# Kernel tuning notes

Hardware: AMD Instinct MI355X
Metric: run time of the kernel (lower is better)

Reference implementation:

```python
import jax, jax.numpy as jnp
import numpy as np

NUM_TERMS = 3
HIDDEN = 64
CLAMP_MIN = 1e-10


def _hermite_basis(x, num_terms):
    hs = [jnp.ones_like(x)]
    if num_terms > 1:
        hs.append(2.0 * x)
    for n in range(1, num_terms - 1):
        hs.append(2.0 * x * hs[n] - 2.0 * n * hs[n - 1])
    return jnp.stack(hs[:num_terms], axis=-1)  # (..., num_terms)


def setup_inputs() -> dict:
    key = jax.random.key(0)
    ks = jax.random.split(key, 7)
    B, S = 2048, 1024
    ys_coeffs = jax.random.normal(ks[0], (B, S, 2), dtype=jnp.float32)
    # scoring MLP params: Linear(3,64) -> ReLU -> Linear(64,64) -> ReLU -> Linear(64,num_terms)
    def lin(k, fan_in, fan_out):
        bound = 1.0 / np.sqrt(fan_in)
        kw, kb = jax.random.split(k)
        W = jax.random.uniform(kw, (fan_in, fan_out), minval=-bound, maxval=bound, dtype=jnp.float32)
        b = jax.random.uniform(kb, (fan_out,), minval=-bound, maxval=bound, dtype=jnp.float32)
        return W, b
    W1, b1 = lin(ks[1], 3, HIDDEN)
    W2, b2 = lin(ks[2], HIDDEN, HIDDEN)
    Wout, bout = lin(ks[3], HIDDEN, NUM_TERMS)
    return {"ys_coeffs": ys_coeffs, "W1": W1, "b1": b1, "W2": W2, "b2": b2,
            "Wout": Wout, "bout": bout}


def reference(ys_coeffs, W1, b1, W2, b2, Wout, bout):
    B, S, _ = ys_coeffs.shape
    timestamps = ys_coeffs[:, :, 0]
    values = ys_coeffs[:, :, 1]
    x0 = values[:, :-1]            # (B, S-1)
    xt = values[:, 1:]             # (B, S-1)
    t = timestamps[:, 1:]          # (B, S-1)
    feats = jnp.stack([xt, t, x0], axis=-1)           # (B, S-1, 3)
    h1 = jax.nn.relu(feats @ W1 + b1)                 # (B, S-1, 64)
    h2 = jax.nn.relu(h1 @ W2 + b2)                    # (B, S-1, 64)
    c_n = h2 @ Wout + bout                            # (B, S-1, num_terms)
    herm = _hermite_basis(xt, NUM_TERMS)              # (B, S-1, num_terms)
    p = jnp.sum(c_n * herm, axis=-1)                  # (B, S-1)
    p = jax.nn.softmax(p, axis=0)                     # softmax over batch dim (as in torch dim=0)
    log_likelihood = jnp.log(jnp.clip(p, CLAMP_MIN)).sum(axis=-1)  # (B,)
    return log_likelihood.mean()
```

## Files before the change

### kernel.cpp

```cpp
#include <hip/hip_runtime.h>
#include <hip/hip_bf16.h>

#define HIDDEN 64
#define BATCH 2048
#define SFULL 1024
#define SM1 1023
#define LN_CLAMP -23.025850929940457f
#define SP_PER 16

typedef __bf16 bf16x8 __attribute__((ext_vector_type(8)));
typedef float  f32x4  __attribute__((ext_vector_type(4)));
typedef float  f32x16 __attribute__((ext_vector_type(16)));

#define FRAG_UNITS 22

__device__ __forceinline__ int sig(int rg) {
    return 16 * ((rg >> 3) & 3) + 8 * ((rg >> 2) & 1) + (rg & 3) + 4 * (rg >> 5);
}

__global__ __launch_bounds__(256) void frag_setup_kernel(
    const float* __restrict__ W1, const float* __restrict__ b1,
    const float* __restrict__ W2, const float* __restrict__ b2,
    const float* __restrict__ Wout, char* __restrict__ F)
{
    const int l    = threadIdx.x & 63;
    const int wv   = threadIdx.x >> 6;
    const int pcol = l & 31;
    const int hi   = l >> 5;

    if (wv == 0) {
#pragma unroll
        for (int mt = 0; mt < 2; ++mt) {
            const int hout = sig(32 * mt + pcol);
            bf16x8 v;
#pragma unroll
            for (int j = 0; j < 8; ++j) {
                const int k = 8 * hi + j;
                v[j] = (k < 3) ? (__bf16)W1[k * 64 + hout]
                     : (k == 3) ? (__bf16)b1[hout] : (__bf16)0.0f;
            }
            *(bf16x8*)(F + ((mt * 64 + l) << 4)) = v;
        }
#pragma unroll
        for (int c = 0; c < 4; ++c) {
            bf16x8 v;
#pragma unroll
            for (int j = 0; j < 8; ++j) {
                const int k = 16 * c + 8 * hi + j;
                v[j] = (pcol < 3) ? (__bf16)Wout[k * 3 + pcol] : (__bf16)0.0f;
            }
            *(bf16x8*)(F + (((10 + c) * 64 + l) << 4)) = v;
        }
    } else if (wv == 1 || wv == 2) {
        const int mt = wv - 1;
        const int hout = sig(32 * mt + pcol);
#pragma unroll
        for (int c = 0; c < 4; ++c) {
            bf16x8 v;
#pragma unroll
            for (int j = 0; j < 8; ++j)
                v[j] = (__bf16)W2[(16 * c + 8 * hi + j) * 64 + hout];
            *(bf16x8*)(F + (((2 + mt * 4 + c) * 64 + l) << 4)) = v;
        }
    } else {
#pragma unroll
        for (int mt = 0; mt < 2; ++mt)
#pragma unroll
            for (int q = 0; q < 4; ++q) {
                f32x4 v;
#pragma unroll
                for (int rr = 0; rr < 4; ++rr) {
                    const int r = 4 * q + rr;
                    v[rr] = b2[16 * (r >> 2) + 8 * hi + (r & 3) + 4 * mt];
                }
                *(f32x4*)(F + (((14 + mt * 4 + q) * 64 + l) << 4)) = v;
            }
    }
}

__global__ __launch_bounds__(256, 3) void mlp_z_kernel(
    const float* __restrict__ ys,
    const char* __restrict__ F,
    const float* __restrict__ bout,
    float* __restrict__ z)
{
    const int l    = threadIdx.x & 63;
    const int wv   = threadIdx.x >> 6;
    const int pcol = l & 31;

    const int b   = (blockIdx.x * 4 + wv) * 32 + pcol;
    const int sp0 = blockIdx.y * SP_PER;
    const int omax = (SFULL - 1) - sp0;

    bf16x8 a1[2], a2[2][4], a3[4];
    f32x16 c2init[2];
#pragma unroll
    for (int mt = 0; mt < 2; ++mt) {
        a1[mt] = *(const bf16x8*)(F + ((mt * 64 + l) << 4));
#pragma unroll
        for (int c = 0; c < 4; ++c)
            a2[mt][c] = *(const bf16x8*)(F + (((2 + mt * 4 + c) * 64 + l) << 4));
#pragma unroll
        for (int q = 0; q < 4; ++q) {
            const f32x4 v = *(const f32x4*)(F + (((14 + mt * 4 + q) * 64 + l) << 4));
            c2init[mt][4 * q + 0] = v[0]; c2init[mt][4 * q + 1] = v[1];
            c2init[mt][4 * q + 2] = v[2]; c2init[mt][4 * q + 3] = v[3];
        }
    }
#pragma unroll
    for (int c = 0; c < 4; ++c)
        a3[c] = *(const bf16x8*)(F + (((10 + c) * 64 + l) << 4));

    const float bo0 = bout[0], bo1 = bout[1], bo2 = bout[2];

    f32x16 zero16;
#pragma unroll
    for (int i = 0; i < 16; ++i) zero16[i] = 0.0f;

    const float2* base2 = reinterpret_cast<const float2*>(ys) + ((size_t)b * SFULL + sp0);
    float* zb = z + (size_t)sp0 * BATCH + b;

    float2 q0 = base2[0];
    float2 q1 = base2[min(1, omax)];
    float2 qn = base2[min(2, omax)];

    for (int it = 0; it < SP_PER; ++it) {
        const float2 qn2 = base2[min(it + 3, omax)];

        const float x0 = q0.y, t = q1.x, xt = q1.y;

        bf16x8 f0;
        f0[0] = (__bf16)xt; f0[1] = (__bf16)t;
        f0[2] = (__bf16)x0; f0[3] = (__bf16)1.0f;
        f0[4] = f0[0]; f0[5] = f0[1]; f0[6] = f0[2]; f0[7] = f0[3];

        f32x16 acc1_0 = __builtin_amdgcn_mfma_f32_32x32x16_bf16(a1[0], f0, zero16, 0, 0, 0);
        f32x16 acc1_1 = __builtin_amdgcn_mfma_f32_32x32x16_bf16(a1[1], f0, zero16, 0, 0, 0);

        bf16x8 h1f[4];
#pragma unroll
        for (int c = 0; c < 4; ++c)
#pragma unroll
            for (int j = 0; j < 4; ++j) {
                h1f[c][j]     = (__bf16)fmaxf(acc1_0[4 * c + j], 0.0f);
                h1f[c][4 + j] = (__bf16)fmaxf(acc1_1[4 * c + j], 0.0f);
            }

        f32x16 acc2_0 = c2init[0];
        f32x16 acc2_1 = c2init[1];
#pragma unroll
        for (int c = 0; c < 4; ++c) {
            acc2_0 = __builtin_amdgcn_mfma_f32_32x32x16_bf16(a2[0][c], h1f[c], acc2_0, 0, 0, 0);
            acc2_1 = __builtin_amdgcn_mfma_f32_32x32x16_bf16(a2[1][c], h1f[c], acc2_1, 0, 0, 0);
        }

        bf16x8 h2f[4];
#pragma unroll
        for (int c = 0; c < 4; ++c)
#pragma unroll
            for (int j = 0; j < 4; ++j) {
                h2f[c][j]     = (__bf16)fmaxf(acc2_0[4 * c + j], 0.0f);
                h2f[c][4 + j] = (__bf16)fmaxf(acc2_1[4 * c + j], 0.0f);
            }

        f32x16 acc3 = zero16;
#pragma unroll
        for (int c = 0; c < 4; ++c)
            acc3 = __builtin_amdgcn_mfma_f32_32x32x16_bf16(a3[c], h2f[c], acc3, 0, 0, 0);

        const float c0 = acc3[0] + bo0;
        const float c1 = acc3[1] + bo1;
        const float c2 = acc3[2] + bo2;
        const float zv = fmaf(c2, fmaf(4.0f * xt, xt, -2.0f),
                         fmaf(c1, xt + xt, c0));

        if (l < 32 && sp0 + it < SM1)
            zb[(size_t)it * BATCH] = zv;

        q0 = q1; q1 = qn; qn = qn2;
    }
}

__device__ __forceinline__ float blk_reduce_max(float v) {
    __shared__ float s[4];
#pragma unroll
    for (int off = 32; off >= 1; off >>= 1) v = fmaxf(v, __shfl_xor(v, off));
    if ((threadIdx.x & 63) == 0) s[threadIdx.x >> 6] = v;
    __syncthreads();
    v = fmaxf(fmaxf(s[0], s[1]), fmaxf(s[2], s[3]));
    __syncthreads();
    return v;
}

__device__ __forceinline__ float blk_reduce_sum(float v) {
    __shared__ float s[4];
#pragma unroll
    for (int off = 32; off >= 1; off >>= 1) v += __shfl_xor(v, off);
    if ((threadIdx.x & 63) == 0) s[threadIdx.x >> 6] = v;
    __syncthreads();
    v = (s[0] + s[1]) + (s[2] + s[3]);
    __syncthreads();
    return v;
}

__global__ __launch_bounds__(256) void col_softmax_kernel(
    const float* __restrict__ z, float* __restrict__ colsum)
{
    const int sp = blockIdx.x;
    const int tid = threadIdx.x;
    const float* col = z + (size_t)sp * BATCH;

    float vals[8];
    float m = -3.4e38f;
#pragma unroll
    for (int i = 0; i < 8; ++i) {
        vals[i] = col[tid + 256 * i];
        m = fmaxf(m, vals[i]);
    }
    const float M = blk_reduce_max(m);

    float se = 0.0f;
#pragma unroll
    for (int i = 0; i < 8; ++i) se += __expf(vals[i] - M);
    const float S = blk_reduce_sum(se);
    const float L = __logf(S);

    float acc = 0.0f;
#pragma unroll
    for (int i = 0; i < 8; ++i) acc += fmaxf(vals[i] - M - L, LN_CLAMP);
    const float T = blk_reduce_sum(acc);
    if (tid == 0) colsum[sp] = T;
}

__global__ __launch_bounds__(256) void final_reduce_kernel(
    const float* __restrict__ colsum, float* __restrict__ out)
{
    const int tid = threadIdx.x;
    float v = 0.0f;
    for (int i = tid; i < SM1; i += 256) v += colsum[i];
    const float T = blk_reduce_sum(v);
    if (tid == 0) out[0] = T / (float)BATCH;
}

extern "C" void kernel_launch(void* const* d_in, const int* in_sizes, int n_in,
                              void* d_out, int out_size, void* d_ws, size_t ws_size,
                              hipStream_t stream) {
    const float* ys   = (const float*)d_in[0];
    const float* W1   = (const float*)d_in[1];
    const float* b1   = (const float*)d_in[2];
    const float* W2   = (const float*)d_in[3];
    const float* b2   = (const float*)d_in[4];
    const float* Wout = (const float*)d_in[5];
    const float* bout = (const float*)d_in[6];
    float* out = (float*)d_out;

    float* z      = (float*)d_ws;
    float* colsum = z + (size_t)SM1 * BATCH;
    size_t fo = ((size_t)SM1 * BATCH + SM1) * sizeof(float);
    fo = (fo + 15) & ~(size_t)15;
    char* F = (char*)d_ws + fo;

    frag_setup_kernel<<<1, 256, 0, stream>>>(W1, b1, W2, b2, Wout, F);
    dim3 grid1(16, 64);
    mlp_z_kernel<<<grid1, 256, 0, stream>>>(ys, F, bout, z);
    col_softmax_kernel<<<SM1, 256, 0, stream>>>(z, colsum);
    final_reduce_kernel<<<1, 256, 0, stream>>>(colsum, out);
}
```

Measured before the change: 48.69 us.

## Interleave two timesteps per iteration and pack bf16 with byte-permute truncation

```diff
diff --git a/kernel.cpp b/kernel.cpp
--- a/kernel.cpp
+++ b/kernel.cpp
@@ -6,7 +6,7 @@
 #define SFULL 1024
 #define SM1 1023
 #define LN_CLAMP -23.025850929940457f
-#define SP_PER 16
+#define PAIRS 8
 
 typedef __bf16 bf16x8 __attribute__((ext_vector_type(8)));
 typedef float  f32x4  __attribute__((ext_vector_type(4)));
@@ -16,6 +16,33 @@
 
 __device__ __forceinline__ int sig(int rg) {
     return 16 * ((rg >> 3) & 3) + 8 * ((rg >> 2) & 1) + (rg & 3) + 4 * (rg >> 5);
+}
+
+__device__ __forceinline__ unsigned pkt(float lo, float hi) {
+    return __builtin_amdgcn_perm(__float_as_uint(hi), __float_as_uint(lo), 0x07060302u);
+}
+__device__ __forceinline__ unsigned rp2(float lo, float hi) {
+    return pkt(fmaxf(lo, 0.0f), fmaxf(hi, 0.0f));
+}
+
+__device__ __forceinline__ void relu_pack4(const f32x16 lo, const f32x16 hi, bf16x8* out) {
+#pragma unroll
+    for (int c = 0; c < 4; ++c) {
+        union { unsigned u[4]; bf16x8 v; } r;
+        r.u[0] = rp2(lo[4 * c + 0], lo[4 * c + 1]);
+        r.u[1] = rp2(lo[4 * c + 2], lo[4 * c + 3]);
+        r.u[2] = rp2(hi[4 * c + 0], hi[4 * c + 1]);
+        r.u[3] = rp2(hi[4 * c + 2], hi[4 * c + 3]);
+        out[c] = r.v;
+    }
+}
+
+__device__ __forceinline__ bf16x8 featpk(float xt, float t, float x0) {
+    union { unsigned u[4]; bf16x8 v; } r;
+    r.u[0] = pkt(xt, t);
+    r.u[1] = pkt(x0, 1.0f);
+    r.u[2] = r.u[0]; r.u[3] = r.u[1];
+    return r.v;
 }
 
 __global__ __launch_bounds__(256) void frag_setup_kernel(
@@ -78,7 +105,7 @@
     }
 }
 
-__global__ __launch_bounds__(256, 3) void mlp_z_kernel(
+__global__ __launch_bounds__(256, 2) void mlp_z_kernel(
     const float* __restrict__ ys,
     const char* __restrict__ F,
     const float* __restrict__ bout,
@@ -89,7 +116,7 @@
     const int pcol = l & 31;
 
     const int b   = (blockIdx.x * 4 + wv) * 32 + pcol;
-    const int sp0 = blockIdx.y * SP_PER;
+    const int sp0 = blockIdx.y * (2 * PAIRS);
     const int omax = (SFULL - 1) - sp0;
 
     bf16x8 a1[2], a2[2][4], a3[4];
@@ -120,64 +147,66 @@
     const float2* base2 = reinterpret_cast<const float2*>(ys) + ((size_t)b * SFULL + sp0);
     float* zb = z + (size_t)sp0 * BATCH + b;
 
-    float2 q0 = base2[0];
-    float2 q1 = base2[min(1, omax)];
-    float2 qn = base2[min(2, omax)];
-
-    for (int it = 0; it < SP_PER; ++it) {
-        const float2 qn2 = base2[min(it + 3, omax)];
-
-        const float x0 = q0.y, t = q1.x, xt = q1.y;
-
-        bf16x8 f0;
-        f0[0] = (__bf16)xt; f0[1] = (__bf16)t;
-        f0[2] = (__bf16)x0; f0[3] = (__bf16)1.0f;
-        f0[4] = f0[0]; f0[5] = f0[1]; f0[6] = f0[2]; f0[7] = f0[3];
-
-        f32x16 acc1_0 = __builtin_amdgcn_mfma_f32_32x32x16_bf16(a1[0], f0, zero16, 0, 0, 0);
-        f32x16 acc1_1 = __builtin_amdgcn_mfma_f32_32x32x16_bf16(a1[1], f0, zero16, 0, 0, 0);
-
-        bf16x8 h1f[4];
-#pragma unroll
-        for (int c = 0; c < 4; ++c)
-#pragma unroll
-            for (int j = 0; j < 4; ++j) {
-                h1f[c][j]     = (__bf16)fmaxf(acc1_0[4 * c + j], 0.0f);
-                h1f[c][4 + j] = (__bf16)fmaxf(acc1_1[4 * c + j], 0.0f);
-            }
-
-        f32x16 acc2_0 = c2init[0];
-        f32x16 acc2_1 = c2init[1];
-#pragma unroll
-        for (int c = 0; c < 4; ++c) {
-            acc2_0 = __builtin_amdgcn_mfma_f32_32x32x16_bf16(a2[0][c], h1f[c], acc2_0, 0, 0, 0);
-            acc2_1 = __builtin_amdgcn_mfma_f32_32x32x16_bf16(a2[1][c], h1f[c], acc2_1, 0, 0, 0);
-        }
-
-        bf16x8 h2f[4];
-#pragma unroll
-        for (int c = 0; c < 4; ++c)
-#pragma unroll
-            for (int j = 0; j < 4; ++j) {
-                h2f[c][j]     = (__bf16)fmaxf(acc2_0[4 * c + j], 0.0f);
-                h2f[c][4 + j] = (__bf16)fmaxf(acc2_1[4 * c + j], 0.0f);
-            }
-
-        f32x16 acc3 = zero16;
-#pragma unroll
-        for (int c = 0; c < 4; ++c)
-            acc3 = __builtin_amdgcn_mfma_f32_32x32x16_bf16(a3[c], h2f[c], acc3, 0, 0, 0);
-
-        const float c0 = acc3[0] + bo0;
-        const float c1 = acc3[1] + bo1;
-        const float c2 = acc3[2] + bo2;
-        const float zv = fmaf(c2, fmaf(4.0f * xt, xt, -2.0f),
-                         fmaf(c1, xt + xt, c0));
-
-        if (l < 32 && sp0 + it < SM1)
-            zb[(size_t)it * BATCH] = zv;
-
-        q0 = q1; q1 = qn; qn = qn2;
+    float2 qa = base2[0];
+    float2 qb = base2[min(1, omax)];
+    float2 qc = base2[min(2, omax)];
+
+    for (int it = 0; it < PAIRS; ++it) {
+        const float2 nb = base2[min(2 * it + 3, omax)];
+        const float2 nc = base2[min(2 * it + 4, omax)];
+
+        const float x0a = qa.y, ta = qb.x, xta = qb.y;
+        const float x0b = qb.y, tb = qc.x, xtb = qc.y;
+
+        const bf16x8 f0a = featpk(xta, ta, x0a);
+        const bf16x8 f0b = featpk(xtb, tb, x0b);
+
+        f32x16 a1_0 = __builtin_amdgcn_mfma_f32_32x32x16_bf16(a1[0], f0a, zero16, 0, 0, 0);
+        f32x16 a1_1 = __builtin_amdgcn_mfma_f32_32x32x16_bf16(a1[1], f0a, zero16, 0, 0, 0);
+        f32x16 b1_0 = __builtin_amdgcn_mfma_f32_32x32x16_bf16(a1[0], f0b, zero16, 0, 0, 0);
+        f32x16 b1_1 = __builtin_amdgcn_mfma_f32_32x32x16_bf16(a1[1], f0b, zero16, 0, 0, 0);
+
+        bf16x8 h1a[4], h1b[4];
+        relu_pack4(a1_0, a1_1, h1a);
+        relu_pack4(b1_0, b1_1, h1b);
+
+        f32x16 a2_0 = __builtin_amdgcn_mfma_f32_32x32x16_bf16(a2[0][0], h1a[0], c2init[0], 0, 0, 0);
+        f32x16 a2_1 = __builtin_amdgcn_mfma_f32_32x32x16_bf16(a2[1][0], h1a[0], c2init[1], 0, 0, 0);
+        f32x16 b2_0 = __builtin_amdgcn_mfma_f32_32x32x16_bf16(a2[0][0], h1b[0], c2init[0], 0, 0, 0);
+        f32x16 b2_1 = __builtin_amdgcn_mfma_f32_32x32x16_bf16(a2[1][0], h1b[0], c2init[1], 0, 0, 0);
+#pragma unroll
+        for (int c = 1; c < 4; ++c) {
+            a2_0 = __builtin_amdgcn_mfma_f32_32x32x16_bf16(a2[0][c], h1a[c], a2_0, 0, 0, 0);
+            a2_1 = __builtin_amdgcn_mfma_f32_32x32x16_bf16(a2[1][c], h1a[c], a2_1, 0, 0, 0);
+            b2_0 = __builtin_amdgcn_mfma_f32_32x32x16_bf16(a2[0][c], h1b[c], b2_0, 0, 0, 0);
+            b2_1 = __builtin_amdgcn_mfma_f32_32x32x16_bf16(a2[1][c], h1b[c], b2_1, 0, 0, 0);
+        }
+
+        bf16x8 h2a[4], h2b[4];
+        relu_pack4(a2_0, a2_1, h2a);
+        relu_pack4(b2_0, b2_1, h2b);
+
+        f32x16 a3acc = __builtin_amdgcn_mfma_f32_32x32x16_bf16(a3[0], h2a[0], zero16, 0, 0, 0);
+        f32x16 b3acc = __builtin_amdgcn_mfma_f32_32x32x16_bf16(a3[0], h2b[0], zero16, 0, 0, 0);
+#pragma unroll
+        for (int c = 1; c < 4; ++c) {
+            a3acc = __builtin_amdgcn_mfma_f32_32x32x16_bf16(a3[c], h2a[c], a3acc, 0, 0, 0);
+            b3acc = __builtin_amdgcn_mfma_f32_32x32x16_bf16(a3[c], h2b[c], b3acc, 0, 0, 0);
+        }
+
+        const float ca0 = a3acc[0] + bo0, ca1 = a3acc[1] + bo1, ca2 = a3acc[2] + bo2;
+        const float cb0 = b3acc[0] + bo0, cb1 = b3acc[1] + bo1, cb2 = b3acc[2] + bo2;
+        const float zva = fmaf(ca2, fmaf(4.0f * xta, xta, -2.0f), fmaf(ca1, xta + xta, ca0));
+        const float zvb = fmaf(cb2, fmaf(4.0f * xtb, xtb, -2.0f), fmaf(cb1, xtb + xtb, cb0));
+
+        if (l < 32) {
+            zb[0] = zva;
+            if (sp0 + 2 * it + 1 < SM1)
+                zb[BATCH] = zvb;
+        }
+        zb += 2 * BATCH;
+
+        qa = qc; qb = nb; qc = nc;
     }
 }
 
```

Result: no change. 48.06 us (-1.3%).
